# Kernel tuning notes

Measured on AMD Instinct MI355X. Metric: run time of the kernel, lower is better.

The kernel has to match this reference:

```python
import jax, jax.numpy as jnp
import numpy as np

D_MODEL = 512
HEADS = 8
WIN = 16
LN_EPS = 1e-5


def setup_inputs() -> dict:
    key = jax.random.key(0)
    ks = jax.random.split(key, 5)
    B, T = 2, 4096
    s = 1.0 / np.sqrt(D_MODEL)
    x = jax.random.normal(ks[0], (B, T, D_MODEL), dtype=jnp.float32)
    Wq = jax.random.normal(ks[1], (D_MODEL, D_MODEL), dtype=jnp.float32) * s
    Wk = jax.random.normal(ks[2], (D_MODEL, D_MODEL), dtype=jnp.float32) * s
    Wv = jax.random.normal(ks[3], (D_MODEL, D_MODEL), dtype=jnp.float32) * s
    Wp = jax.random.normal(ks[4], (D_MODEL, D_MODEL), dtype=jnp.float32) * s
    ln_gamma = jnp.ones((D_MODEL,), dtype=jnp.float32)
    ln_beta = jnp.zeros((D_MODEL,), dtype=jnp.float32)
    return {"x": x, "Wq": Wq, "Wk": Wk, "Wv": Wv, "Wp": Wp,
            "ln_gamma": ln_gamma, "ln_beta": ln_beta}


def _local_attention(x, Wq, Wk, Wv, Wp, ln_gamma, ln_beta):
    B, T, D = x.shape
    H = HEADS
    d = D // H
    scale = d ** (-0.5)
    # projections (torch Linear: y = x @ W^T)
    q = (x @ Wq.T).reshape(B, T, H, d)
    k = (x @ Wk.T).reshape(B, T, H, d)
    v = (x @ Wv.T).reshape(B, T, H, d)
    offs = jnp.arange(-WIN, WIN + 1)                      # [W]
    pos = jnp.arange(T)[:, None] + offs[None, :]          # [T, W]
    valid = (pos >= 0) & (pos < T)                        # [T, W]
    idx = jnp.clip(pos, 0, T - 1)                         # [T, W]
    k_win = k[:, idx]                                     # [B, T, W, H, d]
    v_win = v[:, idx]                                     # [B, T, W, H, d]
    scores = jnp.einsum('bthd,btwhd->bthw', q, k_win) * scale
    scores = jnp.where(valid[None, :, None, :], scores, -jnp.inf)
    attn = jax.nn.softmax(scores, axis=-1)                # over window
    out = jnp.einsum('bthw,btwhd->bthd', attn, v_win).reshape(B, T, D)
    y = x + out @ Wp.T                                    # residual + proj
    mu = jnp.mean(y, axis=-1, keepdims=True)
    var = jnp.mean(jnp.square(y - mu), axis=-1, keepdims=True)
    return ln_gamma * (y - mu) * jax.lax.rsqrt(var + LN_EPS) + ln_beta


def reference(x, Wq, Wk, Wv, Wp, ln_gamma, ln_beta):
    return _local_attention(x, Wq, Wk, Wv, Wp, ln_gamma, ln_beta)
```

## Files before the change

### kernel.cpp

```cpp
#include <hip/hip_runtime.h>
#include <hip/hip_bf16.h>
#include <stdint.h>

typedef __bf16 bf16;
typedef __attribute__((ext_vector_type(8))) __bf16 bf16x8;
typedef __attribute__((ext_vector_type(2))) __bf16 bf16x2;
typedef __attribute__((ext_vector_type(4))) float f32x4;
typedef __attribute__((ext_vector_type(4))) unsigned int u32x4;

#define GLOAD16(gsrc, ldst)                                              \
  __builtin_amdgcn_global_load_lds(                                      \
      (const __attribute__((address_space(1))) unsigned int*)(gsrc),     \
      (__attribute__((address_space(3))) unsigned int*)(ldst), 16, 0, 0)

static constexpr int T_LEN = 4096;
static constexpr int WIN = 16;

__device__ __forceinline__ bf16x8 cvt8(float4 a, float4 b) {
  bf16x8 o;
  o[0] = (bf16)a.x; o[1] = (bf16)a.y; o[2] = (bf16)a.z; o[3] = (bf16)a.w;
  o[4] = (bf16)b.x; o[5] = (bf16)b.y; o[6] = (bf16)b.z; o[7] = (bf16)b.w;
  return o;
}

__global__ __launch_bounds__(256) void prep_kernel(const float* __restrict__ x,
                                                   const float* __restrict__ wq,
                                                   const float* __restrict__ wk,
                                                   const float* __restrict__ wv,
                                                   const float* __restrict__ wp,
                                                   bf16* __restrict__ xb,
                                                   bf16* __restrict__ wqkv,
                                                   bf16* __restrict__ wpb) {
  int bid = blockIdx.x;
  if (bid < 2048) {
    int i = bid * 256 + threadIdx.x;
    const float4* s4 = (const float4*)x + (size_t)i * 2;
    ((bf16x8*)xb)[i] = cvt8(s4[0], s4[1]);
  } else {
    int i = (bid - 2048) * 256 + threadIdx.x;
    int which = i >> 15;
    int j = i & 32767;
    if (which < 3) {
      const float* src = (which == 0) ? wq : (which == 1) ? wk : wv;
      bf16* dst = wqkv + (size_t)which * 512 * 512;
      const float4* s4 = (const float4*)src + (size_t)j * 2;
      ((bf16x8*)dst)[j] = cvt8(s4[0], s4[1]);
    } else {
      int chunk = j >> 9;
      int row = j & 511;
      const float4* s4 = (const float4*)(wp + (size_t)row * 512 + chunk * 8);
      ((bf16x8*)wpb)[j] = cvt8(s4[0], s4[1]);
    }
  }
}

__global__ __launch_bounds__(256) void gemm_qkv_kernel(const bf16* __restrict__ Ab,
                                                       const bf16* __restrict__ Bw,
                                                       bf16* __restrict__ Cb) {
  constexpr int K = 512, BK = 64, NIT = K / BK;
  __shared__ __align__(16) bf16 As[8192];
  __shared__ __align__(16) bf16 Bs[4096];
  const int tid = threadIdx.x;
  const int l = tid & 63;
  const int w = tid >> 6;
  const int g = l >> 4;
  const int c = l & 15;
  int bid = blockIdx.x;
  bid = (bid & 7) * 192 + (bid >> 3);
  const int m0 = (bid / 24) * 128;
  const int n0 = (bid % 24) * 64;

  const int wm = (w >> 1) * 64;
  const int wn = (w & 1) * 32;
  const int cx = c & 7;

  const f32x4 zero = {0.f, 0.f, 0.f, 0.f};
  f32x4 acc[4][2];
#pragma unroll
  for (int i = 0; i < 4; ++i)
#pragma unroll
    for (int j = 0; j < 2; ++j) acc[i][j] = zero;

#pragma unroll 1
  for (int t = 0; t < NIT; ++t) {
    const int k0 = t * BK;
#pragma unroll
    for (int i = 0; i < 4; ++i) {
      int s = tid + i * 256;
      int row = s >> 3;
      int j = s & 7;
      GLOAD16(Ab + (size_t)(m0 + row) * 512 + k0 + ((j ^ (row & 7)) << 3),
              &As[s * 8]);
    }
#pragma unroll
    for (int i = 0; i < 2; ++i) {
      int s = tid + i * 256;
      int row = s >> 3;
      int j = s & 7;
      GLOAD16(Bw + (size_t)(n0 + row) * 512 + k0 + ((j ^ (row & 7)) << 3),
              &Bs[s * 8]);
    }
    __syncthreads();
#pragma unroll
    for (int kk = 0; kk < 2; ++kk) {
      const int joff = ((kk * 4 + g) ^ cx) << 3;
      bf16x8 af[4], bfr[2];
#pragma unroll
      for (int mi = 0; mi < 4; ++mi)
        af[mi] = *(const bf16x8*)&As[(wm + mi * 16 + c) * 64 + joff];
#pragma unroll
      for (int ni = 0; ni < 2; ++ni)
        bfr[ni] = *(const bf16x8*)&Bs[(wn + ni * 16 + c) * 64 + joff];
#pragma unroll
      for (int mi = 0; mi < 4; ++mi)
#pragma unroll
        for (int ni = 0; ni < 2; ++ni)
          acc[mi][ni] = __builtin_amdgcn_mfma_f32_16x16x32_bf16(af[mi], bfr[ni], acc[mi][ni], 0, 0, 0);
    }
    __syncthreads();
  }

  bf16* Cw = &As[w * 2048];
  const int r0 = (l >> 4) * 4;
#pragma unroll
  for (int mi = 0; mi < 4; ++mi)
#pragma unroll
    for (int ni = 0; ni < 2; ++ni)
#pragma unroll
      for (int r = 0; r < 4; ++r)
        Cw[(mi * 16 + r0 + r) * 32 + ni * 16 + c] = (bf16)acc[mi][ni][r];
#pragma unroll
  for (int i = 0; i < 4; ++i) {
    int row = (l >> 2) + 16 * i;
    bf16x8 v = *(const bf16x8*)&Cw[row * 32 + (l & 3) * 8];
    *(bf16x8*)(Cb + (size_t)(m0 + wm + row) * 1536 + n0 + wn + (l & 3) * 8) = v;
  }
}

__global__ __launch_bounds__(512) void attn_proj_ln_kernel(
    const bf16* __restrict__ qkv, const bf16* __restrict__ Bp,
    const float* __restrict__ X, const float* __restrict__ gamma,
    const float* __restrict__ beta, float* __restrict__ out) {
  __shared__ __align__(16) bf16 POOL[63744];
  bf16* KV = POOL;
  bf16* Pp = POOL + 36864;
  bf16* aoutL = POOL + 46080;
  float* rsum = (float*)(POOL + 62720);
  float* rsq  = (float*)(POOL + 63232);

  const int tid = threadIdx.x;
  const int w = tid >> 6;
  const int l = tid & 63;
  const int g = l >> 4;
  const int c = l & 15;
  int bid = blockIdx.x;
  bid = (bid & 7) * 32 + (bid >> 3);
  const int m0 = bid * 32;
  const int b = m0 >> 12;
  const int tloc0 = m0 & (T_LEN - 1);
  const int base = b * T_LEN;

  const f32x4 zero = {0.f, 0.f, 0.f, 0.f};
  const u32x4 zu = {0u, 0u, 0u, 0u};
  const float scale = 0.125f;

  if (tid < 256) {
    int hl = tid >> 6;
    int row = tid & 63;
    *(uint4*)&KV[18432 + hl * 4608 + row * 72 + 64] = make_uint4(0u, 0u, 0u, 0u);
  }

#pragma unroll 1
  for (int pass = 0; pass < 2; ++pass) {
    if (pass) __syncthreads();
#pragma unroll
    for (int i = 0; i < 4; ++i) {
      int task = tid + i * 512;
      int hl = task >> 9;
      int rem = task & 511;
      int pp = rem >> 3;
      int c8 = (rem & 7) * 8;
      int h = pass * 4 + hl;
      int pg = base + min(max(tloc0 - WIN + pp, 0), T_LEN - 1);
      const bf16* kr = qkv + (size_t)pg * 1536 + 512 + h * 64 + c8;
      const bf16* vr = qkv + (size_t)pg * 1536 + 1024 + h * 64 + c8;
      *(bf16x8*)&KV[hl * 4608 + pp * 72 + c8] = *(const bf16x8*)kr;
      bf16x8 vv = *(const bf16x8*)vr;
      bf16* vt = &KV[18432 + hl * 4608];
#pragma unroll
      for (int e = 0; e < 8; ++e)
        vt[(c8 + e) * 72 + pp] = vv[e];
    }
    __syncthreads();

    const int hl = w >> 1;
    const int wh = w & 1;
    const int h = pass * 4 + hl;
    const int tg = tloc0 + wh * 16;
    bf16* Kl = &KV[hl * 4608];
    bf16* Vt = &KV[18432 + hl * 4608];

    const bf16* qrow = qkv + (size_t)(base + tg + c) * 1536 + h * 64;
    bf16x8 qf0 = *(const bf16x8*)(qrow + g * 8);
    bf16x8 qf1 = *(const bf16x8*)(qrow + 32 + g * 8);

    f32x4 st[3];
#pragma unroll
    for (int wt = 0; wt < 3; ++wt) {
      int rk = 16 * wh + 16 * wt + c;
      bf16x8 ka0 = *(const bf16x8*)&Kl[rk * 72 + g * 8];
      bf16x8 ka1 = *(const bf16x8*)&Kl[rk * 72 + 32 + g * 8];
      f32x4 t = __builtin_amdgcn_mfma_f32_16x16x32_bf16(ka0, qf0, zero, 0, 0, 0);
      st[wt] = __builtin_amdgcn_mfma_f32_16x16x32_bf16(ka1, qf1, t, 0, 0, 0);
    }

    float pv[3][4];
    float lsum = 0.f;
#pragma unroll
    for (int wt = 0; wt < 3; ++wt)
#pragma unroll
      for (int r = 0; r < 4; ++r) {
        int ww = 16 * wt + 4 * g + r;
        int pos = tg - WIN + ww;
        bool valid = (ww >= c) && (ww <= c + 32) && (pos >= 0) && (pos < T_LEN);
        float e = __expf(st[wt][r] * scale);
        pv[wt][r] = valid ? e : 0.f;
        lsum += pv[wt][r];
      }
    lsum += __shfl_xor(lsum, 16);
    lsum += __shfl_xor(lsum, 32);
    float inv = 1.f / lsum;

    bf16* P = &Pp[w * 1152];
#pragma unroll
    for (int wt = 0; wt < 3; ++wt) {
      bf16x2 p01, p23;
      p01[0] = (bf16)(pv[wt][0] * inv);
      p01[1] = (bf16)(pv[wt][1] * inv);
      p23[0] = (bf16)(pv[wt][2] * inv);
      p23[1] = (bf16)(pv[wt][3] * inv);
      *(bf16x2*)&P[c * 56 + 16 * wt + 4 * g]     = p01;
      *(bf16x2*)&P[c * 56 + 16 * wt + 4 * g + 2] = p23;
    }

    bf16x8 pa0 = *(const bf16x8*)&P[c * 56 + 8 * g];
    int g1 = (g < 2) ? g : 1;
    bf16x8 pa1 = *(const bf16x8*)&P[c * 56 + 32 + 8 * g1];
    if (g >= 2) pa1 = __builtin_bit_cast(bf16x8, zu);

    const int off0 = 16 * wh + 8 * g;
    const int off1 = 16 * wh + ((g < 2) ? 32 + 8 * g : 48);
    f32x4 acc[4] = {zero, zero, zero, zero};
#pragma unroll
    for (int dt = 0; dt < 4; ++dt) {
      bf16x8 v0 = *(const bf16x8*)&Vt[(16 * dt + c) * 72 + off0];
      bf16x8 v1 = *(const bf16x8*)&Vt[(16 * dt + c) * 72 + off1];
      acc[dt] = __builtin_amdgcn_mfma_f32_16x16x32_bf16(pa0, v0, acc[dt], 0, 0, 0);
      acc[dt] = __builtin_amdgcn_mfma_f32_16x16x32_bf16(pa1, v1, acc[dt], 0, 0, 0);
    }

#pragma unroll
    for (int dt = 0; dt < 4; ++dt)
#pragma unroll
      for (int r = 0; r < 4; ++r)
        aoutL[(wh * 16 + 4 * g + r) * 520 + h * 64 + 16 * dt + c] = (bf16)acc[dt][r];
  }
  __syncthreads();

  f32x4 acc2[2][4];
#pragma unroll
  for (int m = 0; m < 2; ++m)
#pragma unroll
    for (int n = 0; n < 4; ++n) acc2[m][n] = zero;

#pragma unroll
  for (int t = 0; t < 8; ++t) {
#pragma unroll
    for (int kk = 0; kk < 2; ++kk) {
      const int chunk = t * 8 + kk * 4 + g;
      bf16x8 af[2], bfv[4];
#pragma unroll
      for (int m = 0; m < 2; ++m)
        af[m] = *(const bf16x8*)&aoutL[(m * 16 + c) * 520 + chunk * 8];
#pragma unroll
      for (int n = 0; n < 4; ++n)
        bfv[n] = *(const bf16x8*)(Bp + ((size_t)chunk * 512 + w * 64 + n * 16 + c) * 8);
#pragma unroll
      for (int m = 0; m < 2; ++m)
#pragma unroll
        for (int n = 0; n < 4; ++n)
          acc2[m][n] = __builtin_amdgcn_mfma_f32_16x16x32_bf16(af[m], bfv[n], acc2[m][n], 0, 0, 0);
    }
  }

  const int col0 = w * 64 + c;
  float ps[2][4], ps2[2][4];
#pragma unroll
  for (int m = 0; m < 2; ++m)
#pragma unroll
    for (int r = 0; r < 4; ++r) {
      int row = m0 + m * 16 + 4 * g + r;
      float s = 0.f, s2 = 0.f;
#pragma unroll
      for (int n = 0; n < 4; ++n) {
        float y = acc2[m][n][r] + X[(size_t)row * 512 + col0 + n * 16];
        acc2[m][n][r] = y;
        s += y;
        s2 += y * y;
      }
      ps[m][r] = s;
      ps2[m][r] = s2;
    }
#pragma unroll
  for (int m = 0; m < 2; ++m)
#pragma unroll
    for (int r = 0; r < 4; ++r) {
      float s = ps[m][r], s2 = ps2[m][r];
      s += __shfl_xor(s, 1);  s2 += __shfl_xor(s2, 1);
      s += __shfl_xor(s, 2);  s2 += __shfl_xor(s2, 2);
      s += __shfl_xor(s, 4);  s2 += __shfl_xor(s2, 4);
      s += __shfl_xor(s, 8);  s2 += __shfl_xor(s2, 8);
      ps[m][r] = s;
      ps2[m][r] = s2;
    }
  if (c == 0) {
#pragma unroll
    for (int m = 0; m < 2; ++m)
#pragma unroll
      for (int r = 0; r < 4; ++r) {
        rsum[(m * 16 + 4 * g + r) * 8 + w] = ps[m][r];
        rsq[(m * 16 + 4 * g + r) * 8 + w] = ps2[m][r];
      }
  }
  __syncthreads();

  float gam[4], bet[4];
#pragma unroll
  for (int n = 0; n < 4; ++n) {
    gam[n] = gamma[col0 + n * 16];
    bet[n] = beta[col0 + n * 16];
  }
#pragma unroll
  for (int m = 0; m < 2; ++m)
#pragma unroll
    for (int r = 0; r < 4; ++r) {
      int rl = m * 16 + 4 * g + r;
      float sum = 0.f, sq = 0.f;
#pragma unroll
      for (int j = 0; j < 8; ++j) {
        sum += rsum[rl * 8 + j];
        sq += rsq[rl * 8 + j];
      }
      float mu = sum * (1.f / 512.f);
      float var = sq * (1.f / 512.f) - mu * mu;
      float rs = rsqrtf(var + 1e-5f);
#pragma unroll
      for (int n = 0; n < 4; ++n)
        out[(size_t)(m0 + rl) * 512 + col0 + n * 16] =
            gam[n] * (acc2[m][n][r] - mu) * rs + bet[n];
    }
}

extern "C" void kernel_launch(void* const* d_in, const int* in_sizes, int n_in,
                              void* d_out, int out_size, void* d_ws, size_t ws_size,
                              hipStream_t stream) {
  const float* x  = (const float*)d_in[0];
  const float* Wq = (const float*)d_in[1];
  const float* Wk = (const float*)d_in[2];
  const float* Wv = (const float*)d_in[3];
  const float* Wp = (const float*)d_in[4];
  const float* g  = (const float*)d_in[5];
  const float* be = (const float*)d_in[6];
  float* out = (float*)d_out;

  char* ws = (char*)d_ws;
  bf16* xb   = (bf16*)(ws);
  bf16* wqkv = (bf16*)(ws + 8388608);
  bf16* wpb  = (bf16*)(ws + 9961472);
  bf16* qkv  = (bf16*)(ws + 10485760);

  prep_kernel<<<2560, 256, 0, stream>>>(x, Wq, Wk, Wv, Wp, xb, wqkv, wpb);
  gemm_qkv_kernel<<<1536, 256, 0, stream>>>(xb, wqkv, qkv);
  attn_proj_ln_kernel<<<256, 512, 0, stream>>>(qkv, wpb, x, g, be, out);
}
```

Before: 50.77 us.

## Pre-pack operands in MFMA fragment layout and load QKV GEMM directly from global

The prep kernel now writes x and the QKV weights in a chunk-major (k-chunk of 8, then row) layout, so each MFMA fragment becomes one contiguous 16-byte global load. The QKV GEMM drops its LDS staging, swizzling and barriers and reads fragments straight from global memory, keeping LDS only for the output bounce. This removes LDS traffic and synchronisation, but each wave now reloads operands from L2 instead of sharing them through LDS, and there is no explicit prefetch to hide global latency. The x conversion also becomes a transposing write with fewer, larger blocks.

Result: slower. 58.09 us (+14.4%).

```diff
diff --git a/kernel.cpp b/kernel.cpp
--- a/kernel.cpp
+++ b/kernel.cpp
@@ -7,11 +7,6 @@
 typedef __attribute__((ext_vector_type(2))) __bf16 bf16x2;
 typedef __attribute__((ext_vector_type(4))) float f32x4;
 typedef __attribute__((ext_vector_type(4))) unsigned int u32x4;
-
-#define GLOAD16(gsrc, ldst)                                              \
-  __builtin_amdgcn_global_load_lds(                                      \
-      (const __attribute__((address_space(1))) unsigned int*)(gsrc),     \
-      (__attribute__((address_space(3))) unsigned int*)(ldst), 16, 0, 0)
 
 static constexpr int T_LEN = 4096;
 static constexpr int WIN = 16;
@@ -32,34 +27,33 @@
                                                    bf16* __restrict__ wqkv,
                                                    bf16* __restrict__ wpb) {
   int bid = blockIdx.x;
-  if (bid < 2048) {
-    int i = bid * 256 + threadIdx.x;
-    const float4* s4 = (const float4*)x + (size_t)i * 2;
-    ((bf16x8*)xb)[i] = cvt8(s4[0], s4[1]);
+  if (bid < 128) {
+    const int m0 = bid * 64;
+#pragma unroll
+    for (int i = 0; i < 16; ++i) {
+      int s = threadIdx.x + i * 256;
+      int row = s & 63;
+      int chunk = s >> 6;
+      const float4* s4 = (const float4*)(x + (size_t)(m0 + row) * 512 + chunk * 8);
+      ((bf16x8*)xb)[(size_t)chunk * 8192 + m0 + row] = cvt8(s4[0], s4[1]);
+    }
   } else {
-    int i = (bid - 2048) * 256 + threadIdx.x;
+    int i = (bid - 128) * 256 + threadIdx.x;
     int which = i >> 15;
     int j = i & 32767;
-    if (which < 3) {
-      const float* src = (which == 0) ? wq : (which == 1) ? wk : wv;
-      bf16* dst = wqkv + (size_t)which * 512 * 512;
-      const float4* s4 = (const float4*)src + (size_t)j * 2;
-      ((bf16x8*)dst)[j] = cvt8(s4[0], s4[1]);
-    } else {
-      int chunk = j >> 9;
-      int row = j & 511;
-      const float4* s4 = (const float4*)(wp + (size_t)row * 512 + chunk * 8);
-      ((bf16x8*)wpb)[j] = cvt8(s4[0], s4[1]);
-    }
+    int chunk = j >> 9;
+    int row = j & 511;
+    const float* src = (which == 0) ? wq : (which == 1) ? wk : (which == 2) ? wv : wp;
+    bf16* dst = (which < 3) ? (wqkv + (size_t)which * 262144) : wpb;
+    const float4* s4 = (const float4*)(src + (size_t)row * 512 + chunk * 8);
+    ((bf16x8*)dst)[j] = cvt8(s4[0], s4[1]);
   }
 }
 
 __global__ __launch_bounds__(256) void gemm_qkv_kernel(const bf16* __restrict__ Ab,
                                                        const bf16* __restrict__ Bw,
                                                        bf16* __restrict__ Cb) {
-  constexpr int K = 512, BK = 64, NIT = K / BK;
-  __shared__ __align__(16) bf16 As[8192];
-  __shared__ __align__(16) bf16 Bs[4096];
+  __shared__ __align__(16) bf16 Cbounce[8192];
   const int tid = threadIdx.x;
   const int l = tid & 63;
   const int w = tid >> 6;
@@ -69,10 +63,13 @@
   bid = (bid & 7) * 192 + (bid >> 3);
   const int m0 = (bid / 24) * 128;
   const int n0 = (bid % 24) * 64;
+  const int mat = n0 >> 9;
+  const int nr0 = n0 & 511;
 
   const int wm = (w >> 1) * 64;
   const int wn = (w & 1) * 32;
-  const int cx = c & 7;
+
+  const bf16* Bm = Bw + (size_t)mat * 262144;
 
   const f32x4 zero = {0.f, 0.f, 0.f, 0.f};
   f32x4 acc[4][2];
@@ -81,46 +78,29 @@
 #pragma unroll
     for (int j = 0; j < 2; ++j) acc[i][j] = zero;
 
-#pragma unroll 1
-  for (int t = 0; t < NIT; ++t) {
-    const int k0 = t * BK;
-#pragma unroll
-    for (int i = 0; i < 4; ++i) {
-      int s = tid + i * 256;
-      int row = s >> 3;
-      int j = s & 7;
-      GLOAD16(Ab + (size_t)(m0 + row) * 512 + k0 + ((j ^ (row & 7)) << 3),
-              &As[s * 8]);
-    }
-#pragma unroll
-    for (int i = 0; i < 2; ++i) {
-      int s = tid + i * 256;
-      int row = s >> 3;
-      int j = s & 7;
-      GLOAD16(Bw + (size_t)(n0 + row) * 512 + k0 + ((j ^ (row & 7)) << 3),
-              &Bs[s * 8]);
-    }
-    __syncthreads();
+#pragma unroll 2
+  for (int t = 0; t < 8; ++t) {
 #pragma unroll
     for (int kk = 0; kk < 2; ++kk) {
-      const int joff = ((kk * 4 + g) ^ cx) << 3;
+      const int chunk = t * 8 + kk * 4 + g;
       bf16x8 af[4], bfr[2];
 #pragma unroll
       for (int mi = 0; mi < 4; ++mi)
-        af[mi] = *(const bf16x8*)&As[(wm + mi * 16 + c) * 64 + joff];
+        af[mi] = *(const bf16x8*)(Ab +
+            ((size_t)chunk * 8192 + m0 + wm + mi * 16 + c) * 8);
 #pragma unroll
       for (int ni = 0; ni < 2; ++ni)
-        bfr[ni] = *(const bf16x8*)&Bs[(wn + ni * 16 + c) * 64 + joff];
+        bfr[ni] = *(const bf16x8*)(Bm +
+            ((size_t)chunk * 512 + nr0 + wn + ni * 16 + c) * 8);
 #pragma unroll
       for (int mi = 0; mi < 4; ++mi)
 #pragma unroll
         for (int ni = 0; ni < 2; ++ni)
           acc[mi][ni] = __builtin_amdgcn_mfma_f32_16x16x32_bf16(af[mi], bfr[ni], acc[mi][ni], 0, 0, 0);
     }
-    __syncthreads();
-  }
-
-  bf16* Cw = &As[w * 2048];
+  }
+
+  bf16* Cw = &Cbounce[w * 2048];
   const int r0 = (l >> 4) * 4;
 #pragma unroll
   for (int mi = 0; mi < 4; ++mi)
@@ -379,7 +359,7 @@
   bf16* wpb  = (bf16*)(ws + 9961472);
   bf16* qkv  = (bf16*)(ws + 10485760);
 
-  prep_kernel<<<2560, 256, 0, stream>>>(x, Wq, Wk, Wv, Wp, xb, wqkv, wpb);
+  prep_kernel<<<640, 256, 0, stream>>>(x, Wq, Wk, Wv, Wp, xb, wqkv, wpb);
   gemm_qkv_kernel<<<1536, 256, 0, stream>>>(xb, wqkv, qkv);
   attn_proj_ln_kernel<<<256, 512, 0, stream>>>(qkv, wpb, x, g, be, out);
 }
```
